# Performance work log

Hardware: AMD Instinct MI355X
Metric: run time of the kernel (lower is better)

Reference implementation:

```python
import jax, jax.numpy as jnp
import numpy as np

DIM = 96; NH = 3; HD = DIM // NH; SCALE = HD ** -0.5
WS = (7, 7, 7); N = WS[0] * WS[1] * WS[2]
SHIFT = (3, 3, 3)  # half window
NL = 2
GRID = (28, 28, 28)
B = 2


def _rel_index():
    wd, wh, ww = WS
    coords = np.stack(np.meshgrid(np.arange(wd), np.arange(wh), np.arange(ww), indexing='ij')).reshape(3, -1)
    rel = (coords[:, :, None] - coords[:, None, :]).transpose(1, 2, 0)  # [N,N,3]
    rel[..., 0] += wd - 1; rel[..., 1] += wh - 1; rel[..., 2] += ww - 1
    rel[..., 0] *= (2 * wh - 1) * (2 * ww - 1); rel[..., 1] *= (2 * ww - 1)
    return rel.sum(-1)  # [N,N]

REL_IDX = _rel_index()


def _window_partition(x):
    b, D, H, W, C = x.shape
    wd, wh, ww = WS
    x = x.reshape(b, D // wd, wd, H // wh, wh, W // ww, ww, C)
    x = x.transpose(0, 1, 3, 5, 2, 4, 6, 7)
    return x.reshape(-1, N, C)


def _window_reverse(win, b, D, H, W):
    wd, wh, ww = WS
    C = win.shape[-1]
    x = win.reshape(b, D // wd, H // wh, W // ww, wd, wh, ww, C)
    x = x.transpose(0, 1, 4, 2, 5, 3, 6, 7)
    return x.reshape(b, D, H, W, C)


def _compute_mask():
    # MONAI compute_mask for the shifted (SW-MSA) block
    D, H, W = GRID; wd, wh, ww = WS; sd, sh, sw = SHIFT
    img = np.zeros((1, D, H, W, 1), np.float32)
    cnt = 0
    for d in (slice(-wd), slice(-wd, -sd), slice(-sd, None)):
        for h in (slice(-wh), slice(-wh, -sh), slice(-sh, None)):
            for w in (slice(-ww), slice(-ww, -sw), slice(-sw, None)):
                img[:, d, h, w, :] = cnt; cnt += 1
    mw = img.reshape(1, D // wd, wd, H // wh, wh, W // ww, ww, 1)
    mw = mw.transpose(0, 1, 3, 5, 2, 4, 6, 7).reshape(-1, N)  # [nw, N]
    am = mw[:, None, :] - mw[:, :, None]
    return np.where(am != 0, np.float32(-100.0), np.float32(0.0))

MASK = jnp.asarray(_compute_mask())  # [nw, N, N]


def _ln(x, g, b):
    mu = x.mean(-1, keepdims=True)
    var = ((x - mu) ** 2).mean(-1, keepdims=True)
    return (x - mu) / jnp.sqrt(var + 1e-5) * g + b


def _block(x, p, shift, mask):
    b, D, H, W, C = x.shape
    h = _ln(x, p['n1g'], p['n1b'])
    if shift is not None:
        h = jnp.roll(h, (-shift[0], -shift[1], -shift[2]), axis=(1, 2, 3))
    xw = _window_partition(h)  # [b*nw, N, C]
    Bn = xw.shape[0]
    qkv = (xw @ p['qkvw'].T + p['qkvb']).reshape(Bn, N, 3, NH, HD).transpose(2, 0, 3, 1, 4)
    q, k, v = qkv[0] * SCALE, qkv[1], qkv[2]
    attn = jnp.einsum('bhnd,bhmd->bhnm', q, k)
    bias = p['rel'][REL_IDX.reshape(-1)].reshape(N, N, NH).transpose(2, 0, 1)
    attn = attn + bias[None]
    if mask is not None:
        nw = mask.shape[0]
        attn = (attn.reshape(Bn // nw, nw, NH, N, N) + mask[None, :, None]).reshape(Bn, NH, N, N)
    attn = jax.nn.softmax(attn, axis=-1)
    out = jnp.einsum('bhnm,bhmd->bhnd', attn, v).transpose(0, 2, 1, 3).reshape(Bn, N, C)
    out = out @ p['projw'].T + p['projb']
    h = _window_reverse(out, b, D, H, W)
    if shift is not None:
        h = jnp.roll(h, shift, axis=(1, 2, 3))
    x = x + h
    m = _ln(x, p['n2g'], p['n2b'])
    m = jax.nn.gelu(m @ p['fc1w'].T + p['fc1b'], approximate=False) @ p['fc2w'].T + p['fc2b']
    return x + m


def setup_inputs() -> dict:
    key = jax.random.key(0)
    ks = jax.random.split(key, 8)
    nbias = (2 * WS[0] - 1) * (2 * WS[1] - 1) * (2 * WS[2] - 1)
    return {
        'x': jax.random.normal(ks[0], (B,) + GRID + (DIM,), jnp.float32),
        'norm1_g': jnp.ones((NL, DIM), jnp.float32),
        'norm1_b': jnp.zeros((NL, DIM), jnp.float32),
        'qkv_w': jax.random.normal(ks[1], (NL, 3 * DIM, DIM), jnp.float32) * 0.02,
        'qkv_b': jnp.zeros((NL, 3 * DIM), jnp.float32),
        'rel_bias': jax.random.normal(ks[2], (NL, nbias, NH), jnp.float32) * 0.02,
        'proj_w': jax.random.normal(ks[3], (NL, DIM, DIM), jnp.float32) * 0.02,
        'proj_b': jnp.zeros((NL, DIM), jnp.float32),
        'norm2_g': jnp.ones((NL, DIM), jnp.float32),
        'norm2_b': jnp.zeros((NL, DIM), jnp.float32),
        'fc1_w': jax.random.normal(ks[4], (NL, 4 * DIM, DIM), jnp.float32) * 0.02,
        'fc1_b': jnp.zeros((NL, 4 * DIM), jnp.float32),
        'fc2_w': jax.random.normal(ks[5], (NL, DIM, 4 * DIM), jnp.float32) * 0.02,
        'fc2_b': jnp.zeros((NL, DIM), jnp.float32),
    }


def reference(x, norm1_g, norm1_b, qkv_w, qkv_b, rel_bias, proj_w, proj_b,
              norm2_g, norm2_b, fc1_w, fc1_b, fc2_w, fc2_b):
    for i in range(NL):
        p = dict(n1g=norm1_g[i], n1b=norm1_b[i], qkvw=qkv_w[i], qkvb=qkv_b[i],
                 rel=rel_bias[i], projw=proj_w[i], projb=proj_b[i],
                 n2g=norm2_g[i], n2b=norm2_b[i], fc1w=fc1_w[i], fc1b=fc1_b[i],
                 fc2w=fc2_w[i], fc2b=fc2_b[i])
        if i % 2 == 0:
            x = _block(x, p, None, None)  # W-MSA (mask is all-zero for shift=0)
        else:
            x = _block(x, p, SHIFT, MASK)  # SW-MSA
    return x
```

## Files before the change

kernel.cpp:

```cpp
#include <hip/hip_runtime.h>
#include <math.h>

#define DIM 96
#define NHD 3
#define HD 32
#define NWT 343
#define NWIN 128
#define TOK 43904
#define NBIAS 2197
#define SCALE 0.17677669529663687f
#define TPAD 352
#define TSZ  (343 * 352)

typedef __attribute__((ext_vector_type(8))) short bf16x8;
typedef __attribute__((ext_vector_type(4))) float f32x4;

__device__ __forceinline__ unsigned short f2b(float f) {
    union { float f; unsigned int u; } x; x.f = f;
    unsigned int r = (x.u + 0x7fffu + ((x.u >> 16) & 1u)) >> 16;
    return (unsigned short)r;
}
__device__ __forceinline__ unsigned int pk2bf(float a, float b) {
    union { float f; unsigned int u; } x, y; x.f = a; y.f = b;
    return ((x.u + 0x8000u) >> 16) | ((y.u + 0x8000u) & 0xffff0000u);
}

__global__ void __launch_bounds__(256) k_cvt4(
        const float* __restrict__ s0, const float* __restrict__ s1,
        const float* __restrict__ s2, const float* __restrict__ s3,
        unsigned short* __restrict__ dst) {
    int i = blockIdx.x * 256 + threadIdx.x;
    if (i >= 221184) return;
    const float* src; int off;
    if (i < 55296)       { src = s0; off = i; }
    else if (i < 73728)  { src = s1; off = i - 55296; }
    else if (i < 147456) { src = s2; off = i - 73728; }
    else                 { src = s3; off = i - 147456; }
    dst[i] = f2b(src[off]);
}

__global__ void __launch_bounds__(256) k_bias(
        const float* __restrict__ rel0, const float* __restrict__ rel1,
        float* __restrict__ bt) {
    int i = blockIdx.x * 256 + threadIdx.x;
    if (i >= 9 * 3 * 343 * 352) return;
    int kcol = i % 352;
    int t = i / 352;
    int q = t % 343; t /= 343;
    int head = t % 3; int combo = t / 3;
    float outv;
    if (kcol >= 343) {
        outv = -100000.0f;
    } else {
        int dq = q / 49, hq = (q / 7) % 7, wq = q % 7;
        int dk = kcol / 49, hk = (kcol / 7) % 7, wk = kcol % 7;
        int ridx = (dq - dk + 6) * 169 + (hq - hk + 6) * 13 + (wq - wk + 6);
        const float* rel = (combo == 0) ? rel0 : rel1;
        float b = rel[ridx * 3 + head];
        if (combo > 0) {
            int ty = combo - 1;
            int rqd = (ty & 4) ? 1 + (dq >= 4) : 0;
            int rqh = (ty & 2) ? 1 + (hq >= 4) : 0;
            int rqw = (ty & 1) ? 1 + (wq >= 4) : 0;
            int rkd = (ty & 4) ? 1 + (dk >= 4) : 0;
            int rkh = (ty & 2) ? 1 + (hk >= 4) : 0;
            int rkw = (ty & 1) ? 1 + (wk >= 4) : 0;
            if (rqd != rkd || rqh != rkh || rqw != rkw) b -= 100.0f;
        }
        outv = b;
    }
    bt[i] = outv;
}

__global__ void __launch_bounds__(256) k_qkv(
        const float* __restrict__ x, const float* __restrict__ g1,
        const float* __restrict__ b1, const unsigned short* __restrict__ W,
        const float* __restrict__ bias, unsigned short* __restrict__ q,
        unsigned short* __restrict__ k, unsigned short* __restrict__ v, int shift) {
    __shared__ __align__(16) unsigned short lns[64][104];
    __shared__ __align__(16) unsigned short wbuf[96][104];
    int wid = threadIdx.x >> 6, lane = threadIdx.x & 63;
    int lm = lane & 15, q4 = lane >> 4;
    int m0 = blockIdx.x * 64 + wid * 16;
    int bwr[4], nnr[4];
    size_t rowoff[4];
    #pragma unroll
    for (int r = 0; r < 4; ++r) {
        int wtok = m0 + q4 * 4 + r;
        int bw = wtok / NWT, n = wtok % NWT;
        bwr[r] = bw; nnr[r] = n;
        int b = bw >> 6, win = bw & 63;
        int wdi = win >> 4, whi = (win >> 2) & 3, wwi = win & 3;
        int d = n / 49, h = (n / 7) % 7, w = n % 7;
        int sd = (wdi * 7 + d + shift) % 28;
        int sh = (whi * 7 + h + shift) % 28;
        int sw = (wwi * 7 + w + shift) % 28;
        rowoff[r] = (((size_t)(b * 28 + sd) * 28 + sh) * 28 + sw) * 96;
    }
    float val[6][4], g1v[6], b1v[6];
    #pragma unroll
    for (int c = 0; c < 6; ++c) {
        int ncol = c * 16 + lm;
        g1v[c] = g1[ncol]; b1v[c] = b1[ncol];
        #pragma unroll
        for (int r = 0; r < 4; ++r) val[c][r] = x[rowoff[r] + ncol];
    }
    #pragma unroll
    for (int r = 0; r < 4; ++r) {
        float s = 0.f, s2 = 0.f;
        #pragma unroll
        for (int c = 0; c < 6; ++c) { s += val[c][r]; s2 += val[c][r] * val[c][r]; }
        #pragma unroll
        for (int off = 8; off > 0; off >>= 1) {
            s  += __shfl_xor(s,  off, 64);
            s2 += __shfl_xor(s2, off, 64);
        }
        float mu = s * (1.0f / 96.0f);
        float rstd = rsqrtf(s2 * (1.0f / 96.0f) - mu * mu + 1e-5f);
        int row = wid * 16 + q4 * 4 + r;
        #pragma unroll
        for (int c = 0; c < 6; ++c)
            lns[row][c * 16 + lm] = f2b((val[c][r] - mu) * rstd * g1v[c] + b1v[c]);
    }
    __syncthreads();
    bf16x8 a1[3];
    #pragma unroll
    for (int ks = 0; ks < 3; ++ks)
        a1[ks] = *((const bf16x8*)&lns[wid * 16 + lm][ks * 32 + q4 * 8]);
    for (int ch = 0; ch < 3; ++ch) {
        __syncthreads();
        const uint4* src = (const uint4*)(W + ch * 96 * 96);
        for (int s = threadIdx.x; s < 1152; s += 256) {
            int row = s / 12, seg = s % 12;
            *((uint4*)&wbuf[row][seg * 8]) = src[s];
        }
        __syncthreads();
        f32x4 acc[6];
        #pragma unroll
        for (int c = 0; c < 6; ++c) acc[c] = (f32x4){0.f, 0.f, 0.f, 0.f};
        #pragma unroll
        for (int ks = 0; ks < 3; ++ks) {
            #pragma unroll
            for (int c = 0; c < 6; ++c) {
                bf16x8 b = *((const bf16x8*)&wbuf[c * 16 + lm][ks * 32 + q4 * 8]);
                acc[c] = __builtin_amdgcn_mfma_f32_16x16x32_bf16(a1[ks], b, acc[c], 0, 0, 0);
            }
        }
        #pragma unroll
        for (int c = 0; c < 6; ++c) {
            int col = c * 16 + lm;
            int head = col >> 5, hd = col & 31;
            float bb = bias[ch * 96 + col];
            #pragma unroll
            for (int r = 0; r < 4; ++r) {
                int wh = bwr[r] * NHD + head;
                float vv = acc[c][r] + bb;
                if (ch == 0)
                    q[(size_t)wh * (TPAD * 32) + nnr[r] * 32 + hd] = f2b(vv * SCALE);
                else if (ch == 1)
                    k[(size_t)wh * (TPAD * 32) + nnr[r] * 32 + hd] = f2b(vv);
                else
                    v[(size_t)wh * (32 * TPAD) + hd * TPAD + nnr[r]] = f2b(vv);
            }
        }
    }
}

__global__ void __launch_bounds__(256) k_attn(
        const unsigned short* __restrict__ q, const unsigned short* __restrict__ k,
        const unsigned short* __restrict__ vT, const float* __restrict__ bt,
        unsigned short* __restrict__ o, int tmul) {
    __shared__ __align__(16) unsigned short vts[32 * 360];
    __shared__ __align__(16) unsigned short pbuf[4][2][16 * 40];
    __shared__ float dnm[4][2][16];
    int wh = blockIdx.x / 3, third = blockIdx.x % 3;
    int bw = wh / NHD, head = wh % NHD;
    const unsigned int* vsrc = (const unsigned int*)(vT + (size_t)wh * 32 * TPAD);
    unsigned int* vdst = (unsigned int*)vts;
    for (int i = threadIdx.x; i < 32 * 176; i += 256) {
        int row = i / 176, cc = i - row * 176;
        vdst[row * 180 + cc] = vsrc[i];
    }
    __syncthreads();
    int win = bw & 63;
    int wdi = win >> 4, whi = (win >> 2) & 3, wwi = win & 3;
    int type = ((wdi == 3) ? 4 : 0) | ((whi == 3) ? 2 : 0) | ((wwi == 3) ? 1 : 0);
    const float* bbase = bt + (size_t)type * tmul + (size_t)head * TSZ;
    int wid = threadIdx.x >> 6, lane = threadIdx.x & 63;
    int lm = lane & 15, q4 = lane >> 4;
    int tb = third * 8 + wid * 2;
    if (tb > 21) return;
    bool dual = (tb + 1 <= 21);
    int qtA = tb, qtB = dual ? tb + 1 : tb;
    const unsigned short* qbase = q + (size_t)wh * TPAD * 32;
    const unsigned short* kbase = k + (size_t)wh * TPAD * 32;
    int qtokA = qtA * 16 + lm, qtokB = qtB * 16 + lm;
    bf16x8 qfA = *((const bf16x8*)(qbase + qtokA * 32 + q4 * 8));
    bf16x8 qfB = *((const bf16x8*)(qbase + qtokB * 32 + q4 * 8));
    const float* bpA = bbase + (size_t)min(qtokA, NWT - 1) * 352;
    const float* bpB = bbase + (size_t)min(qtokB, NWT - 1) * 352;
    f32x4 aA0 = (f32x4){0.f,0.f,0.f,0.f}, aA1 = aA0, aB0 = aA0, aB1 = aA0;
    float dA = 0.f, dB = 0.f;
    unsigned short* pbA = pbuf[wid][0];
    unsigned short* pbB = pbuf[wid][1];
    for (int pr = 0; pr < 11; ++pr) {
        int kb0 = pr * 32;
        bf16x8 kf0 = *((const bf16x8*)(kbase + (kb0 + lm) * 32 + q4 * 8));
        bf16x8 kf1 = *((const bf16x8*)(kbase + (kb0 + 16 + lm) * 32 + q4 * 8));
        f32x4 bA0 = *((const f32x4*)(bpA + kb0 + q4 * 4));
        f32x4 bA1 = *((const f32x4*)(bpA + kb0 + 16 + q4 * 4));
        f32x4 bB0 = *((const f32x4*)(bpB + kb0 + q4 * 4));
        f32x4 bB1 = *((const f32x4*)(bpB + kb0 + 16 + q4 * 4));
        f32x4 z = (f32x4){0.f, 0.f, 0.f, 0.f};
        f32x4 sA0 = __builtin_amdgcn_mfma_f32_16x16x32_bf16(kf0, qfA, z, 0, 0, 0);
        f32x4 sA1 = __builtin_amdgcn_mfma_f32_16x16x32_bf16(kf1, qfA, z, 0, 0, 0);
        f32x4 sB0 = __builtin_amdgcn_mfma_f32_16x16x32_bf16(kf0, qfB, z, 0, 0, 0);
        f32x4 sB1 = __builtin_amdgcn_mfma_f32_16x16x32_bf16(kf1, qfB, z, 0, 0, 0);
        float pA[8], pB[8];
        #pragma unroll
        for (int r = 0; r < 4; ++r) {
            float a0 = __expf(sA0[r] + bA0[r]); dA += a0; pA[r] = a0;
            float a1 = __expf(sA1[r] + bA1[r]); dA += a1; pA[4 + r] = a1;
            float b0 = __expf(sB0[r] + bB0[r]); dB += b0; pB[r] = b0;
            float b1 = __expf(sB1[r] + bB1[r]); dB += b1; pB[4 + r] = b1;
        }
        #pragma unroll
        for (int t = 0; t < 2; ++t) {
            *((unsigned int*)(pbA + lm * 40 + t * 16 + q4 * 4)) =
                pk2bf(pA[t * 4 + 0], pA[t * 4 + 1]);
            *((unsigned int*)(pbA + lm * 40 + t * 16 + q4 * 4 + 2)) =
                pk2bf(pA[t * 4 + 2], pA[t * 4 + 3]);
            *((unsigned int*)(pbB + lm * 40 + t * 16 + q4 * 4)) =
                pk2bf(pB[t * 4 + 0], pB[t * 4 + 1]);
            *((unsigned int*)(pbB + lm * 40 + t * 16 + q4 * 4 + 2)) =
                pk2bf(pB[t * 4 + 2], pB[t * 4 + 3]);
        }
        bf16x8 pfA = *((const bf16x8*)(pbA + lm * 40 + q4 * 8));
        bf16x8 pfB = *((const bf16x8*)(pbB + lm * 40 + q4 * 8));
        bf16x8 v0 = *((const bf16x8*)(vts + lm * 360 + kb0 + q4 * 8));
        bf16x8 v1 = *((const bf16x8*)(vts + (16 + lm) * 360 + kb0 + q4 * 8));
        aA0 = __builtin_amdgcn_mfma_f32_16x16x32_bf16(pfA, v0, aA0, 0, 0, 0);
        aA1 = __builtin_amdgcn_mfma_f32_16x16x32_bf16(pfA, v1, aA1, 0, 0, 0);
        aB0 = __builtin_amdgcn_mfma_f32_16x16x32_bf16(pfB, v0, aB0, 0, 0, 0);
        aB1 = __builtin_amdgcn_mfma_f32_16x16x32_bf16(pfB, v1, aB1, 0, 0, 0);
    }
    dA += __shfl_xor(dA, 16, 64); dA += __shfl_xor(dA, 32, 64);
    dB += __shfl_xor(dB, 16, 64); dB += __shfl_xor(dB, 32, 64);
    if (lane < 16) { dnm[wid][0][lm] = dA; dnm[wid][1][lm] = dB; }
    #pragma unroll
    for (int r = 0; r < 4; ++r) {
        int qrowA = qtA * 16 + q4 * 4 + r;
        if (qrowA < NWT) {
            float inv = 1.0f / dnm[wid][0][q4 * 4 + r];
            unsigned short* op = o + (size_t)(bw * NWT + qrowA) * DIM + head * HD;
            op[lm]      = f2b(aA0[r] * inv);
            op[16 + lm] = f2b(aA1[r] * inv);
        }
    }
    if (dual) {
        #pragma unroll
        for (int r = 0; r < 4; ++r) {
            int qrowB = qtB * 16 + q4 * 4 + r;
            if (qrowB < NWT) {
                float inv = 1.0f / dnm[wid][1][q4 * 4 + r];
                unsigned short* op = o + (size_t)(bw * NWT + qrowB) * DIM + head * HD;
                op[lm]      = f2b(aB0[r] * inv);
                op[16 + lm] = f2b(aB1[r] * inv);
            }
        }
    }
}

__global__ void __launch_bounds__(256) k_pm(
        const unsigned short* __restrict__ ao, const unsigned short* __restrict__ Wp,
        const float* __restrict__ pbias, const float* __restrict__ xin,
        float* __restrict__ xout,
        const float* __restrict__ g2, const float* __restrict__ b2,
        const unsigned short* __restrict__ w1, const float* __restrict__ bb1,
        const unsigned short* __restrict__ w2, const float* __restrict__ bb2,
        int shift) {
    __shared__ __align__(16) unsigned short lns[64][104];
    __shared__ __align__(16) unsigned short big[18816];
    int wid = threadIdx.x >> 6, lane = threadIdx.x & 63;
    int lm = lane & 15, q4 = lane >> 4;
    int m0 = blockIdx.x * 64 + wid * 16;
    for (int s = threadIdx.x; s < 1152; s += 256) {
        int row = s / 12, seg = s % 12;
        *((uint4*)&big[row * 104 + seg * 8]) = ((const uint4*)Wp)[s];
    }
    const unsigned short* arow = ao + (size_t)(m0 + lm) * 96;
    bf16x8 a1[3];
    #pragma unroll
    for (int ks = 0; ks < 3; ++ks)
        a1[ks] = *((const bf16x8*)(arow + ks * 32 + q4 * 8));
    __syncthreads();
    f32x4 acc[6];
    #pragma unroll
    for (int c = 0; c < 6; ++c) acc[c] = (f32x4){0.f, 0.f, 0.f, 0.f};
    #pragma unroll
    for (int ks = 0; ks < 3; ++ks) {
        #pragma unroll
        for (int c = 0; c < 6; ++c) {
            bf16x8 b = *((const bf16x8*)&big[(c * 16 + lm) * 104 + ks * 32 + q4 * 8]);
            acc[c] = __builtin_amdgcn_mfma_f32_16x16x32_bf16(a1[ks], b, acc[c], 0, 0, 0);
        }
    }
    size_t rowoff[4];
    #pragma unroll
    for (int r = 0; r < 4; ++r) {
        int wtok = m0 + q4 * 4 + r;
        int bw = wtok / NWT, n = wtok % NWT;
        int b = bw >> 6, win = bw & 63;
        int wdi = win >> 4, whi = (win >> 2) & 3, wwi = win & 3;
        int d = n / 49, h = (n / 7) % 7, w = n % 7;
        int sd = (wdi * 7 + d + shift) % 28;
        int sh = (whi * 7 + h + shift) % 28;
        int sw = (wwi * 7 + w + shift) % 28;
        rowoff[r] = (((size_t)(b * 28 + sd) * 28 + sh) * 28 + sw) * 96;
    }
    float val[6][4], g2v[6], b2v[6];
    #pragma unroll
    for (int c = 0; c < 6; ++c) {
        int n = c * 16 + lm;
        float bb = pbias[n];
        g2v[c] = g2[n]; b2v[c] = b2[n];
        #pragma unroll
        for (int r = 0; r < 4; ++r)
            val[c][r] = xin[rowoff[r] + n] + acc[c][r] + bb;
    }
    #pragma unroll
    for (int r = 0; r < 4; ++r) {
        float s = 0.f, s2 = 0.f;
        #pragma unroll
        for (int c = 0; c < 6; ++c) { s += val[c][r]; s2 += val[c][r] * val[c][r]; }
        #pragma unroll
        for (int off = 8; off > 0; off >>= 1) {
            s  += __shfl_xor(s,  off, 64);
            s2 += __shfl_xor(s2, off, 64);
        }
        float mu = s * (1.0f / 96.0f);
        float rstd = rsqrtf(s2 * (1.0f / 96.0f) - mu * mu + 1e-5f);
        int row = wid * 16 + q4 * 4 + r;
        #pragma unroll
        for (int c = 0; c < 6; ++c)
            lns[row][c * 16 + lm] = f2b((val[c][r] - mu) * rstd * g2v[c] + b2v[c]);
    }
    bf16x8 am[3];
    #pragma unroll
    for (int ks = 0; ks < 3; ++ks)
        am[ks] = *((const bf16x8*)&lns[wid * 16 + lm][ks * 32 + q4 * 8]);
    f32x4 acc2[6];
    #pragma unroll
    for (int c = 0; c < 6; ++c) acc2[c] = (f32x4){0.f, 0.f, 0.f, 0.f};
    unsigned short* hid_ = &big[13952 + wid * 1216];
    for (int ch = 0; ch < 6; ++ch) {
        __syncthreads();
        const uint4* src1 = (const uint4*)(w1 + ch * 64 * 96);
        #pragma unroll
        for (int t = 0; t < 3; ++t) {
            int s = threadIdx.x + t * 256;
            int row = s / 12, seg = s % 12;
            *((uint4*)&big[row * 104 + seg * 8]) = src1[s];
        }
        #pragma unroll
        for (int t = 0; t < 3; ++t) {
            int s = threadIdx.x + t * 256;
            int row = s >> 3, seg = s & 7;
            *((uint4*)&big[6656 + row * 76 + seg * 8]) =
                *((const uint4*)(w2 + row * 384 + ch * 64 + seg * 8));
        }
        __syncthreads();
        f32x4 acc1[4];
        #pragma unroll
        for (int t = 0; t < 4; ++t) acc1[t] = (f32x4){0.f, 0.f, 0.f, 0.f};
        #pragma unroll
        for (int ks = 0; ks < 3; ++ks) {
            #pragma unroll
            for (int t = 0; t < 4; ++t) {
                bf16x8 b = *((const bf16x8*)&big[(t * 16 + lm) * 104 + ks * 32 + q4 * 8]);
                acc1[t] = __builtin_amdgcn_mfma_f32_16x16x32_bf16(am[ks], b, acc1[t], 0, 0, 0);
            }
        }
        #pragma unroll
        for (int t = 0; t < 4; ++t) {
            float bb = bb1[ch * 64 + t * 16 + lm];
            #pragma unroll
            for (int r = 0; r < 4; ++r) {
                float v2 = acc1[t][r] + bb;
                float ge = 0.5f * v2 * (1.0f + erff(v2 * 0.70710678118654752f));
                hid_[(q4 * 4 + r) * 76 + t * 16 + lm] = f2b(ge);
            }
        }
        #pragma unroll
        for (int ks2 = 0; ks2 < 2; ++ks2) {
            bf16x8 a = *((const bf16x8*)(hid_ + lm * 76 + ks2 * 32 + q4 * 8));
            #pragma unroll
            for (int c = 0; c < 6; ++c) {
                bf16x8 b = *((const bf16x8*)&big[6656 + (c * 16 + lm) * 76 + ks2 * 32 + q4 * 8]);
                acc2[c] = __builtin_amdgcn_mfma_f32_16x16x32_bf16(a, b, acc2[c], 0, 0, 0);
            }
        }
    }
    #pragma unroll
    for (int c = 0; c < 6; ++c) {
        int n = c * 16 + lm;
        float bb = bb2[n];
        #pragma unroll
        for (int r = 0; r < 4; ++r)
            xout[rowoff[r] + n] = val[c][r] + acc2[c][r] + bb;
    }
}

extern "C" void kernel_launch(void* const* d_in, const int* in_sizes, int n_in,
                              void* d_out, int out_size, void* d_ws, size_t ws_size,
                              hipStream_t stream) {
    const float* x     = (const float*)d_in[0];
    const float* n1g   = (const float*)d_in[1];
    const float* n1b   = (const float*)d_in[2];
    const float* qkvw  = (const float*)d_in[3];
    const float* qkvb  = (const float*)d_in[4];
    const float* relb  = (const float*)d_in[5];
    const float* projw = (const float*)d_in[6];
    const float* projb = (const float*)d_in[7];
    const float* n2g   = (const float*)d_in[8];
    const float* n2b   = (const float*)d_in[9];
    const float* fc1w  = (const float*)d_in[10];
    const float* fc1b  = (const float*)d_in[11];
    const float* fc2w  = (const float*)d_in[12];
    const float* fc2b  = (const float*)d_in[13];
    float* out = (float*)d_out;

    const size_t NEL = (size_t)TOK * DIM;
    const size_t QKN = (size_t)NWIN * NHD * TPAD * 32;
    float* buf_x = (float*)d_ws;
    unsigned short* hbuf = (unsigned short*)(buf_x + NEL);
    unsigned short* bq   = hbuf + NEL;
    unsigned short* bk   = bq + QKN;
    unsigned short* bv   = bk + QKN;
    unsigned short* wts  = bv + QKN;
    unsigned short* wq  = wts;
    unsigned short* wp  = wq + 2 * 27648;
    unsigned short* w1  = wp + 2 * 9216;
    unsigned short* w2  = w1 + 2 * 36864;
    float* btab = (float*)(wts + 221184);

    k_cvt4<<<(221184 + 255) / 256, 256, 0, stream>>>(qkvw, projw, fc1w, fc2w, wts);
    k_bias<<<(9 * 3 * 343 * 352 + 255) / 256, 256, 0, stream>>>(
        relb, relb + NBIAS * NHD, btab);

    for (int L = 0; L < 2; ++L) {
        int shift = (L == 0) ? 0 : 3;
        const float* xin_l = (L == 0) ? x : buf_x;
        float* xfin = (L == 0) ? buf_x : out;
        const float* btL = (L == 0) ? btab : btab + 3 * TSZ;
        int tmul = (L == 0) ? 0 : 3 * TSZ;

        k_qkv<<<TOK / 64, 256, 0, stream>>>(xin_l, n1g + L * 96, n1b + L * 96,
                                            wq + L * 27648, qkvb + L * 288,
                                            bq, bk, bv, shift);
        k_attn<<<NWIN * NHD * 3, 256, 0, stream>>>(bq, bk, bv, btL, hbuf, tmul);
        k_pm<<<TOK / 64, 256, 0, stream>>>(hbuf, wp + L * 9216, projb + L * 96,
                                           xin_l, xfin,
                                           n2g + L * 96, n2b + L * 96,
                                           w1 + L * 36864, fc1b + L * 384,
                                           w2 + L * 36864, fc2b + L * 96, shift);
    }
}
```

Measured before the change: 291.2 us.

## Store attention bias table as bf16 in MFMA order, prefetch K/bias tiles

The precomputed relative-position/mask bias table is stored in bf16 instead of fp32. Its columns are permuted so each lane fetches its eight bias values with one 16-byte load. The attention loop software-prefetches the next K fragments and bias vectors one iteration ahead, and the softmax denominator moves to a lane shuffle instead of shared memory. This halves bias-table traffic and hides load latency, at the cost of bf16 rounding of the bias (-100 mask values become coarser) and a few more live registers.

```diff
diff --git a/kernel.cpp b/kernel.cpp
--- a/kernel.cpp
+++ b/kernel.cpp
@@ -23,6 +23,12 @@
 __device__ __forceinline__ unsigned int pk2bf(float a, float b) {
     union { float f; unsigned int u; } x, y; x.f = a; y.f = b;
     return ((x.u + 0x8000u) >> 16) | ((y.u + 0x8000u) & 0xffff0000u);
+}
+__device__ __forceinline__ float lo16(unsigned int u) {
+    union { unsigned int u; float f; } x; x.u = u << 16; return x.f;
+}
+__device__ __forceinline__ float hi16(unsigned int u) {
+    union { unsigned int u; float f; } x; x.u = u & 0xffff0000u; return x.f;
 }
 
 __global__ void __launch_bounds__(256) k_cvt4(
@@ -41,13 +47,15 @@
 
 __global__ void __launch_bounds__(256) k_bias(
         const float* __restrict__ rel0, const float* __restrict__ rel1,
-        float* __restrict__ bt) {
+        unsigned short* __restrict__ bt) {
     int i = blockIdx.x * 256 + threadIdx.x;
-    if (i >= 9 * 3 * 343 * 352) return;
-    int kcol = i % 352;
+    if (i >= 9 * 3 * TSZ) return;
+    int c = i % 352;
     int t = i / 352;
     int q = t % 343; t /= 343;
     int head = t % 3; int combo = t / 3;
+    int j = c & 7, q4i = (c >> 3) & 3, pr = c >> 5;
+    int kcol = pr * 32 + ((j >> 2) << 4) + q4i * 4 + (j & 3);
     float outv;
     if (kcol >= 343) {
         outv = -100000.0f;
@@ -69,7 +77,7 @@
         }
         outv = b;
     }
-    bt[i] = outv;
+    bt[i] = f2b(outv);
 }
 
 __global__ void __launch_bounds__(256) k_qkv(
@@ -168,11 +176,10 @@
 
 __global__ void __launch_bounds__(256) k_attn(
         const unsigned short* __restrict__ q, const unsigned short* __restrict__ k,
-        const unsigned short* __restrict__ vT, const float* __restrict__ bt,
+        const unsigned short* __restrict__ vT, const unsigned short* __restrict__ bt,
         unsigned short* __restrict__ o, int tmul) {
     __shared__ __align__(16) unsigned short vts[32 * 360];
     __shared__ __align__(16) unsigned short pbuf[4][2][16 * 40];
-    __shared__ float dnm[4][2][16];
     int wh = blockIdx.x / 3, third = blockIdx.x % 3;
     int bw = wh / NHD, head = wh % NHD;
     const unsigned int* vsrc = (const unsigned int*)(vT + (size_t)wh * 32 * TPAD);
@@ -185,7 +192,7 @@
     int win = bw & 63;
     int wdi = win >> 4, whi = (win >> 2) & 3, wwi = win & 3;
     int type = ((wdi == 3) ? 4 : 0) | ((whi == 3) ? 2 : 0) | ((wwi == 3) ? 1 : 0);
-    const float* bbase = bt + (size_t)type * tmul + (size_t)head * TSZ;
+    const unsigned short* bbase = bt + (size_t)type * tmul + (size_t)head * TSZ;
     int wid = threadIdx.x >> 6, lane = threadIdx.x & 63;
     int lm = lane & 15, q4 = lane >> 4;
     int tb = third * 8 + wid * 2;
@@ -197,33 +204,43 @@
     int qtokA = qtA * 16 + lm, qtokB = qtB * 16 + lm;
     bf16x8 qfA = *((const bf16x8*)(qbase + qtokA * 32 + q4 * 8));
     bf16x8 qfB = *((const bf16x8*)(qbase + qtokB * 32 + q4 * 8));
-    const float* bpA = bbase + (size_t)min(qtokA, NWT - 1) * 352;
-    const float* bpB = bbase + (size_t)min(qtokB, NWT - 1) * 352;
+    const unsigned short* bpA = bbase + (size_t)min(qtokA, NWT - 1) * 352;
+    const unsigned short* bpB = bbase + (size_t)min(qtokB, NWT - 1) * 352;
     f32x4 aA0 = (f32x4){0.f,0.f,0.f,0.f}, aA1 = aA0, aB0 = aA0, aB1 = aA0;
     float dA = 0.f, dB = 0.f;
     unsigned short* pbA = pbuf[wid][0];
     unsigned short* pbB = pbuf[wid][1];
+    bf16x8 kf0n = *((const bf16x8*)(kbase + lm * 32 + q4 * 8));
+    bf16x8 kf1n = *((const bf16x8*)(kbase + (16 + lm) * 32 + q4 * 8));
+    uint4 bAn = *((const uint4*)(bpA + q4 * 8));
+    uint4 bBn = *((const uint4*)(bpB + q4 * 8));
     for (int pr = 0; pr < 11; ++pr) {
         int kb0 = pr * 32;
-        bf16x8 kf0 = *((const bf16x8*)(kbase + (kb0 + lm) * 32 + q4 * 8));
-        bf16x8 kf1 = *((const bf16x8*)(kbase + (kb0 + 16 + lm) * 32 + q4 * 8));
-        f32x4 bA0 = *((const f32x4*)(bpA + kb0 + q4 * 4));
-        f32x4 bA1 = *((const f32x4*)(bpA + kb0 + 16 + q4 * 4));
-        f32x4 bB0 = *((const f32x4*)(bpB + kb0 + q4 * 4));
-        f32x4 bB1 = *((const f32x4*)(bpB + kb0 + 16 + q4 * 4));
+        bf16x8 kf0 = kf0n, kf1 = kf1n;
+        uint4 uA = bAn, uB = bBn;
+        if (pr < 10) {
+            int kb1 = kb0 + 32;
+            kf0n = *((const bf16x8*)(kbase + (kb1 + lm) * 32 + q4 * 8));
+            kf1n = *((const bf16x8*)(kbase + (kb1 + 16 + lm) * 32 + q4 * 8));
+            bAn = *((const uint4*)(bpA + kb1 + q4 * 8));
+            bBn = *((const uint4*)(bpB + kb1 + q4 * 8));
+        }
         f32x4 z = (f32x4){0.f, 0.f, 0.f, 0.f};
         f32x4 sA0 = __builtin_amdgcn_mfma_f32_16x16x32_bf16(kf0, qfA, z, 0, 0, 0);
         f32x4 sA1 = __builtin_amdgcn_mfma_f32_16x16x32_bf16(kf1, qfA, z, 0, 0, 0);
         f32x4 sB0 = __builtin_amdgcn_mfma_f32_16x16x32_bf16(kf0, qfB, z, 0, 0, 0);
         f32x4 sB1 = __builtin_amdgcn_mfma_f32_16x16x32_bf16(kf1, qfB, z, 0, 0, 0);
         float pA[8], pB[8];
-        #pragma unroll
-        for (int r = 0; r < 4; ++r) {
-            float a0 = __expf(sA0[r] + bA0[r]); dA += a0; pA[r] = a0;
-            float a1 = __expf(sA1[r] + bA1[r]); dA += a1; pA[4 + r] = a1;
-            float b0 = __expf(sB0[r] + bB0[r]); dB += b0; pB[r] = b0;
-            float b1 = __expf(sB1[r] + bB1[r]); dB += b1; pB[4 + r] = b1;
-        }
+        pA[0] = __expf(sA0[0] + lo16(uA.x)); pA[1] = __expf(sA0[1] + hi16(uA.x));
+        pA[2] = __expf(sA0[2] + lo16(uA.y)); pA[3] = __expf(sA0[3] + hi16(uA.y));
+        pA[4] = __expf(sA1[0] + lo16(uA.z)); pA[5] = __expf(sA1[1] + hi16(uA.z));
+        pA[6] = __expf(sA1[2] + lo16(uA.w)); pA[7] = __expf(sA1[3] + hi16(uA.w));
+        pB[0] = __expf(sB0[0] + lo16(uB.x)); pB[1] = __expf(sB0[1] + hi16(uB.x));
+        pB[2] = __expf(sB0[2] + lo16(uB.y)); pB[3] = __expf(sB0[3] + hi16(uB.y));
+        pB[4] = __expf(sB1[0] + lo16(uB.z)); pB[5] = __expf(sB1[1] + hi16(uB.z));
+        pB[6] = __expf(sB1[2] + lo16(uB.w)); pB[7] = __expf(sB1[3] + hi16(uB.w));
+        #pragma unroll
+        for (int j = 0; j < 8; ++j) { dA += pA[j]; dB += pB[j]; }
         #pragma unroll
         for (int t = 0; t < 2; ++t) {
             *((unsigned int*)(pbA + lm * 40 + t * 16 + q4 * 4)) =
@@ -246,12 +263,11 @@
     }
     dA += __shfl_xor(dA, 16, 64); dA += __shfl_xor(dA, 32, 64);
     dB += __shfl_xor(dB, 16, 64); dB += __shfl_xor(dB, 32, 64);
-    if (lane < 16) { dnm[wid][0][lm] = dA; dnm[wid][1][lm] = dB; }
     #pragma unroll
     for (int r = 0; r < 4; ++r) {
         int qrowA = qtA * 16 + q4 * 4 + r;
         if (qrowA < NWT) {
-            float inv = 1.0f / dnm[wid][0][q4 * 4 + r];
+            float inv = 1.0f / __shfl(dA, q4 * 4 + r, 64);
             unsigned short* op = o + (size_t)(bw * NWT + qrowA) * DIM + head * HD;
             op[lm]      = f2b(aA0[r] * inv);
             op[16 + lm] = f2b(aA1[r] * inv);
@@ -262,7 +278,7 @@
         for (int r = 0; r < 4; ++r) {
             int qrowB = qtB * 16 + q4 * 4 + r;
             if (qrowB < NWT) {
-                float inv = 1.0f / dnm[wid][1][q4 * 4 + r];
+                float inv = 1.0f / __shfl(dB, q4 * 4 + r, 64);
                 unsigned short* op = o + (size_t)(bw * NWT + qrowB) * DIM + head * HD;
                 op[lm]      = f2b(aB0[r] * inv);
                 op[16 + lm] = f2b(aB1[r] * inv);
@@ -442,17 +458,17 @@
     unsigned short* wp  = wq + 2 * 27648;
     unsigned short* w1  = wp + 2 * 9216;
     unsigned short* w2  = w1 + 2 * 36864;
-    float* btab = (float*)(wts + 221184);
+    unsigned short* btab = wts + 221184;
 
     k_cvt4<<<(221184 + 255) / 256, 256, 0, stream>>>(qkvw, projw, fc1w, fc2w, wts);
-    k_bias<<<(9 * 3 * 343 * 352 + 255) / 256, 256, 0, stream>>>(
+    k_bias<<<(9 * 3 * TSZ + 255) / 256, 256, 0, stream>>>(
         relb, relb + NBIAS * NHD, btab);
 
     for (int L = 0; L < 2; ++L) {
         int shift = (L == 0) ? 0 : 3;
         const float* xin_l = (L == 0) ? x : buf_x;
         float* xfin = (L == 0) ? buf_x : out;
-        const float* btL = (L == 0) ? btab : btab + 3 * TSZ;
+        const unsigned short* btL = (L == 0) ? btab : btab + 3 * TSZ;
         int tmul = (L == 0) ? 0 : 3 * TSZ;
 
         k_qkv<<<TOK / 64, 256, 0, stream>>>(xin_l, n1g + L * 96, n1b + L * 96,
```

Result: faster. 261.4 us (-10.2%).
